# Kernel tuning notes

Measured on AMD Instinct MI355X. Metric: run time of the kernel, lower is better.

Reference implementation:

```python
import jax, jax.numpy as jnp
import numpy as np

B, L = 4096, 200
G_DIM, L_DIM, A_DIM, H = 64, 64, 8, 32
MAX_ACTION = 1.0


def _init(k, shape, fan_in):
    bound = 1.0 / np.sqrt(fan_in)
    return jax.random.uniform(k, shape, jnp.float32, -bound, bound)


def setup_inputs() -> dict:
    key = jax.random.key(0)
    ks = jax.random.split(key, 16)
    return dict(
        global_states=jax.random.normal(ks[0], (B, G_DIM), jnp.float32),
        local_states=jax.random.normal(ks[1], (B, L, L_DIM), jnp.float32),
        W_w=_init(ks[2], (H, G_DIM), G_DIM), W_b=_init(ks[3], (H,), G_DIM),
        U_w=_init(ks[4], (H, L_DIM), L_DIM), U_b=_init(ks[5], (H,), L_DIM),
        att_w=_init(ks[6], (1, 2 * H), 2 * H), att_b=_init(ks[7], (1,), 2 * H),
        l1_w=_init(ks[8], (256, 2 * H), 2 * H), l1_b=_init(ks[9], (256,), 2 * H),
        l2_w=_init(ks[10], (256, 256), 256), l2_b=_init(ks[11], (256,), 256),
        l3_w=_init(ks[12], (A_DIM, 256), 256), l3_b=_init(ks[13], (A_DIM,), 256),
    )


def reference(global_states, local_states, W_w, W_b, U_w, U_b,
              att_w, att_b, l1_w, l1_b, l2_w, l2_b, l3_w, l3_b):
    h = W_w.shape[0]  # 32
    wg = global_states @ W_w.T + W_b                              # [B,H]
    ul = jnp.einsum('bld,hd->blh', local_states, U_w) + U_b       # [B,L,H]
    # att input row0 = cat(wg, wg); rows 1..L = cat(wg, ul)
    a_g, a_l = att_w[0, :h], att_w[0, h:]
    g_term = wg @ a_g                                             # [B]
    s0 = jax.nn.leaky_relu(g_term + wg @ a_l + att_b[0])          # [B]
    sl = jax.nn.leaky_relu(g_term[:, None] + ul @ a_l + att_b[0]) # [B,L]
    # normalize by sum (not softmax), matching torch.div(score, score.sum())
    total = s0 + sl.sum(axis=1)                                   # [B]
    n0 = s0 / total                                               # [B]
    nl = sl / total[:, None]                                      # [B,L]
    agg_local = jnp.einsum('bl,blh->bh', nl, ul)                  # [B,H]
    states = jax.nn.relu(jnp.concatenate([n0[:, None] * wg, agg_local], axis=1))  # [B,2H]
    a = jax.nn.relu(states @ l1_w.T + l1_b)
    a = jax.nn.relu(a @ l2_w.T + l2_b)
    a = jax.nn.sigmoid(a @ l3_w.T + l3_b)
    return MAX_ACTION * a
```

## Files before the change

kernel.cpp:

```cpp
#include <hip/hip_runtime.h>
#include <math.h>

#define BB 4096
#define LL 200
#define GD 64
#define HH 32
#define LPAD 207
#define RR 8

__global__ __launch_bounds__(256) void stage1_kernel(
    const float* __restrict__ gs,
    const float* __restrict__ ls,
    const float* __restrict__ W_w,
    const float* __restrict__ W_b,
    const float* __restrict__ U_w,
    const float* __restrict__ U_b,
    const float* __restrict__ att_w,
    const float* __restrict__ att_b,
    float* __restrict__ states)
{
    __shared__ float xT[64 * LPAD];
    __shared__ float s_wg[HH];
    __shared__ float s_misc[2];
    __shared__ float s_V[HH + 1];

    const int tid = threadIdx.x;
    const int b   = blockIdx.x;

    const float2* ls2 = (const float2*)(ls + (size_t)b * (LL * 64));
    for (int i = tid; i < LL * 32; i += 256) {
        float2 v = ls2[i];
        int d2 = i & 31;
        int l  = i >> 5;
        xT[(2 * d2 + 0) * LPAD + l] = v.x;
        xT[(2 * d2 + 1) * LPAD + l] = v.y;
    }

    if (tid < HH) {
        float acc = W_b[tid];
        const float* g = gs + (size_t)b * GD;
        #pragma unroll
        for (int d = 0; d < GD; ++d)
            acc += g[d] * W_w[tid * GD + d];
        s_wg[tid] = acc;
    }
    __syncthreads();

    const int lx = (tid < LL) ? tid : (LL - 1);
    float x[64];
    #pragma unroll
    for (int d = 0; d < 64; ++d)
        x[d] = xT[d * LPAD + lx];

    if (tid == 0) {
        float gt = 0.f, t2 = 0.f;
        #pragma unroll
        for (int h = 0; h < HH; ++h) {
            gt += s_wg[h] * att_w[h];
            t2 += s_wg[h] * att_w[HH + h];
        }
        float lin = gt + t2 + att_b[0];
        s_misc[0] = gt;
        s_misc[1] = (lin > 0.f) ? lin : 0.01f * lin;
    }
    __syncthreads();

    float* red = xT;
    float t = 0.f;
    for (int h = 0; h < HH; ++h) {
        float acc = U_b[h];
        #pragma unroll
        for (int d = 0; d < 64; ++d)
            acc += x[d] * U_w[h * 64 + d];
        t += acc * att_w[HH + h];
        red[tid * 33 + h] = acc;
    }
    float gt  = s_misc[0];
    float lin = gt + t + att_b[0];
    float sl  = (lin > 0.f) ? lin : 0.01f * lin;
    if (tid >= LL) sl = 0.f;
    red[tid * 33 + 32] = sl;
    __syncthreads();

    if (tid <= HH) {
        float s = 0.f;
        for (int tt = 0; tt < 256; ++tt) {
            float m = (tid < HH) ? red[tt * 33 + tid] : 1.f;
            s += m * red[tt * 33 + 32];
        }
        s_V[tid] = s;
    }
    __syncthreads();

    if (tid < 64) {
        float s0    = s_misc[1];
        float total = s0 + s_V[HH];
        float v;
        if (tid < HH) v = (s0 / total) * s_wg[tid];
        else          v = s_V[tid - HH] / total;
        states[(size_t)b * 64 + tid] = fmaxf(v, 0.f);
    }
}

__global__ __launch_bounds__(256) void mlp_kernel(
    const float* __restrict__ states,
    const float* __restrict__ l1_w, const float* __restrict__ l1_b,
    const float* __restrict__ l2_w, const float* __restrict__ l2_b,
    const float* __restrict__ l3_w, const float* __restrict__ l3_b,
    float* __restrict__ out)
{
    __shared__ __align__(16) float s_x [RR * 64];
    __shared__ __align__(16) float s_a1[RR * 256];
    __shared__ float s_a2[RR * 257];

    const int tid = threadIdx.x;
    const int b0  = blockIdx.x * RR;

    const float4* st4 = (const float4*)(states + (size_t)b0 * 64);
    if (tid < RR * 16) ((float4*)s_x)[tid] = st4[tid];
    __syncthreads();

    float w[64];

    {
        const float* wr = l1_w + tid * 64;
        #pragma unroll
        for (int d = 0; d < 64; ++d) w[d] = wr[d];
        float bias = l1_b[tid];
        #pragma unroll
        for (int r = 0; r < RR; ++r) {
            float acc = bias;
            #pragma unroll
            for (int d = 0; d < 64; ++d)
                acc += s_x[r * 64 + d] * w[d];
            s_a1[r * 256 + tid] = fmaxf(acc, 0.f);
        }
    }
    __syncthreads();

    {
        float acc[RR];
        float bias = l2_b[tid];
        #pragma unroll
        for (int r = 0; r < RR; ++r) acc[r] = bias;
        for (int kc = 0; kc < 4; ++kc) {
            const float* wr = l2_w + tid * 256 + kc * 64;
            #pragma unroll
            for (int d = 0; d < 64; ++d) w[d] = wr[d];
            #pragma unroll
            for (int r = 0; r < RR; ++r) {
                #pragma unroll
                for (int d = 0; d < 64; ++d)
                    acc[r] += s_a1[r * 256 + kc * 64 + d] * w[d];
            }
        }
        #pragma unroll
        for (int r = 0; r < RR; ++r)
            s_a2[r * 257 + tid] = fmaxf(acc[r], 0.f);
    }
    __syncthreads();

    if (tid < RR * 8) {
        int r = tid >> 3, o = tid & 7;
        float acc = l3_b[o];
        const float* wr = l3_w + o * 256;
        #pragma unroll 8
        for (int k = 0; k < 256; ++k)
            acc += s_a2[r * 257 + k] * wr[k];
        out[(size_t)(b0 + r) * 8 + o] = 1.f / (1.f + expf(-acc));
    }
}

extern "C" void kernel_launch(void* const* d_in, const int* in_sizes, int n_in,
                              void* d_out, int out_size, void* d_ws, size_t ws_size,
                              hipStream_t stream)
{
    const float* gs    = (const float*)d_in[0];
    const float* ls    = (const float*)d_in[1];
    const float* W_w   = (const float*)d_in[2];
    const float* W_b   = (const float*)d_in[3];
    const float* U_w   = (const float*)d_in[4];
    const float* U_b   = (const float*)d_in[5];
    const float* att_w = (const float*)d_in[6];
    const float* att_b = (const float*)d_in[7];
    const float* l1_w  = (const float*)d_in[8];
    const float* l1_b  = (const float*)d_in[9];
    const float* l2_w  = (const float*)d_in[10];
    const float* l2_b  = (const float*)d_in[11];
    const float* l3_w  = (const float*)d_in[12];
    const float* l3_b  = (const float*)d_in[13];

    float* states = (float*)d_ws;
    float* out    = (float*)d_out;

    stage1_kernel<<<BB, 256, 0, stream>>>(gs, ls, W_w, W_b, U_w, U_b,
                                          att_w, att_b, states);
    mlp_kernel<<<BB / RR, 256, 0, stream>>>(states, l1_w, l1_b, l2_w, l2_b,
                                            l3_w, l3_b, out);
}
```

Before: 410.8 us.

## Fold attention weights into U and aggregate raw inputs before projecting

The stage-1 kernel is rewritten to use the linearity of the U projection. It precomputes c = a_l·U_w so each score needs only a 64-wide dot product, accumulates the score-weighted sum of raw local states, and applies U_w once per batch row. Each wave now handles one batch row with float4 streaming loads, software prefetch and shuffle reductions, which replaces the shared-memory transpose and the per-position 32x64 projection. The MLP row tile RR is also lowered from 8 to 4, which doubles the number of MLP blocks but reloads the weights more often per row.

```diff
diff --git a/kernel.cpp b/kernel.cpp
--- a/kernel.cpp
+++ b/kernel.cpp
@@ -3,10 +3,8 @@
 
 #define BB 4096
 #define LL 200
-#define GD 64
 #define HH 32
-#define LPAD 207
-#define RR 8
+#define RR 4
 
 __global__ __launch_bounds__(256) void stage1_kernel(
     const float* __restrict__ gs,
@@ -19,87 +17,107 @@
     const float* __restrict__ att_b,
     float* __restrict__ states)
 {
-    __shared__ float xT[64 * LPAD];
-    __shared__ float s_wg[HH];
-    __shared__ float s_misc[2];
-    __shared__ float s_V[HH + 1];
-
-    const int tid = threadIdx.x;
-    const int b   = blockIdx.x;
-
-    const float2* ls2 = (const float2*)(ls + (size_t)b * (LL * 64));
-    for (int i = tid; i < LL * 32; i += 256) {
-        float2 v = ls2[i];
-        int d2 = i & 31;
-        int l  = i >> 5;
-        xT[(2 * d2 + 0) * LPAD + l] = v.x;
-        xT[(2 * d2 + 1) * LPAD + l] = v.y;
-    }
-
-    if (tid < HH) {
-        float acc = W_b[tid];
-        const float* g = gs + (size_t)b * GD;
-        #pragma unroll
-        for (int d = 0; d < GD; ++d)
-            acc += g[d] * W_w[tid * GD + d];
-        s_wg[tid] = acc;
-    }
-    __syncthreads();
-
-    const int lx = (tid < LL) ? tid : (LL - 1);
-    float x[64];
-    #pragma unroll
-    for (int d = 0; d < 64; ++d)
-        x[d] = xT[d * LPAD + lx];
-
-    if (tid == 0) {
-        float gt = 0.f, t2 = 0.f;
-        #pragma unroll
-        for (int h = 0; h < HH; ++h) {
-            gt += s_wg[h] * att_w[h];
-            t2 += s_wg[h] * att_w[HH + h];
-        }
-        float lin = gt + t2 + att_b[0];
-        s_misc[0] = gt;
-        s_misc[1] = (lin > 0.f) ? lin : 0.01f * lin;
-    }
-    __syncthreads();
-
-    float* red = xT;
-    float t = 0.f;
-    for (int h = 0; h < HH; ++h) {
-        float acc = U_b[h];
-        #pragma unroll
-        for (int d = 0; d < 64; ++d)
-            acc += x[d] * U_w[h * 64 + d];
-        t += acc * att_w[HH + h];
-        red[tid * 33 + h] = acc;
-    }
-    float gt  = s_misc[0];
-    float lin = gt + t + att_b[0];
-    float sl  = (lin > 0.f) ? lin : 0.01f * lin;
-    if (tid >= LL) sl = 0.f;
-    red[tid * 33 + 32] = sl;
-    __syncthreads();
-
-    if (tid <= HH) {
-        float s = 0.f;
-        for (int tt = 0; tt < 256; ++tt) {
-            float m = (tid < HH) ? red[tt * 33 + tid] : 1.f;
-            s += m * red[tt * 33 + 32];
-        }
-        s_V[tid] = s;
-    }
-    __syncthreads();
-
-    if (tid < 64) {
-        float s0    = s_misc[1];
-        float total = s0 + s_V[HH];
-        float v;
-        if (tid < HH) v = (s0 / total) * s_wg[tid];
-        else          v = s_V[tid - HH] / total;
-        states[(size_t)b * 64 + tid] = fmaxf(v, 0.f);
-    }
+    __shared__ float c_lds[4 * 64];
+    __shared__ float y_lds[4 * 64];
+
+    const int tid  = threadIdx.x;
+    const int lane = tid & 63;
+    const int wid  = tid >> 6;
+    const int b    = blockIdx.x * 4 + wid;
+
+    const int h    = lane & 31;
+    const int half = lane >> 5;
+    const int q    = lane & 15;
+    const int lg   = lane >> 4;
+
+    const float4* g4 = (const float4*)(gs + (size_t)b * 64);
+    const float4* W4 = (const float4*)(W_w);
+    float wg = (half == 0) ? W_b[h] : 0.f;
+    #pragma unroll
+    for (int dd = 0; dd < 8; ++dd) {
+        float4 gv = g4[half * 8 + dd];
+        float4 wv = W4[h * 16 + half * 8 + dd];
+        wg += gv.x * wv.x + gv.y * wv.y + gv.z * wv.z + gv.w * wv.w;
+    }
+    wg += __shfl_xor(wg, 32);
+
+    float gt = wg * att_w[h];
+    float t2 = wg * att_w[HH + h];
+    #pragma unroll
+    for (int m = 1; m < 32; m <<= 1) {
+        gt += __shfl_xor(gt, m);
+        t2 += __shfl_xor(t2, m);
+    }
+    const float attb = att_b[0];
+    const float lin0 = gt + t2 + attb;
+    const float s0   = (lin0 > 0.f) ? lin0 : 0.01f * lin0;
+
+    float c = 0.f;
+    float ubal = 0.f;
+    #pragma unroll
+    for (int hh = 0; hh < HH; ++hh) {
+        const float alh = att_w[HH + hh];
+        c    += alh * U_w[hh * 64 + lane];
+        ubal += alh * U_b[hh];
+    }
+    c_lds[wid * 64 + lane] = c;
+    __syncthreads();
+    const float4 cq = *(const float4*)&c_lds[wid * 64 + 4 * q];
+    const float base = gt + ubal + attb;
+
+    const float4* xs = (const float4*)(ls + (size_t)b * (LL * 64));
+    const int idx0 = lg * 16 + q;
+    float4 yx = make_float4(0.f, 0.f, 0.f, 0.f);
+    float Sacc = 0.f;
+    float4 X0 = xs[idx0];
+    float4 X1 = xs[idx0 + 64];
+    #pragma unroll 2
+    for (int t = 0; t < 50; ++t) {
+        float4 X = X0;
+        X0 = X1;
+        const int tn = (t + 2 < 50) ? (t + 2) : 49;
+        X1 = xs[idx0 + tn * 64];
+
+        float p = X.x * cq.x + X.y * cq.y + X.z * cq.z + X.w * cq.w;
+        p += __shfl_xor(p, 1);
+        p += __shfl_xor(p, 2);
+        p += __shfl_xor(p, 4);
+        p += __shfl_xor(p, 8);
+        const float linv = p + base;
+        const float sl = (linv > 0.f) ? linv : 0.01f * linv;
+        yx.x += sl * X.x;
+        yx.y += sl * X.y;
+        yx.z += sl * X.z;
+        yx.w += sl * X.w;
+        Sacc += sl;
+    }
+
+    #pragma unroll
+    for (int m = 16; m < 64; m <<= 1) {
+        yx.x += __shfl_xor(yx.x, m);
+        yx.y += __shfl_xor(yx.y, m);
+        yx.z += __shfl_xor(yx.z, m);
+        yx.w += __shfl_xor(yx.w, m);
+        Sacc += __shfl_xor(Sacc, m);
+    }
+    if (lane < 16) *(float4*)&y_lds[wid * 64 + 4 * q] = yx;
+    __syncthreads();
+
+    float V = (half == 0) ? (U_b[h] * Sacc) : 0.f;
+    const float4* U4 = (const float4*)U_w;
+    const float4* y4 = (const float4*)&y_lds[wid * 64];
+    #pragma unroll
+    for (int dd = 0; dd < 8; ++dd) {
+        float4 uv = U4[h * 16 + half * 8 + dd];
+        float4 yv = y4[half * 8 + dd];
+        V += uv.x * yv.x + uv.y * yv.y + uv.z * yv.z + uv.w * yv.w;
+    }
+    V += __shfl_xor(V, 32);
+
+    const float total = s0 + Sacc;
+    const float n0    = s0 / total;
+    const float outv  = (lane < 32) ? (n0 * wg) : (V / total);
+    states[(size_t)b * 64 + lane] = fmaxf(outv, 0.f);
 }
 
 __global__ __launch_bounds__(256) void mlp_kernel(
@@ -193,8 +211,8 @@
     float* states = (float*)d_ws;
     float* out    = (float*)d_out;
 
-    stage1_kernel<<<BB, 256, 0, stream>>>(gs, ls, W_w, W_b, U_w, U_b,
-                                          att_w, att_b, states);
+    stage1_kernel<<<BB / 4, 256, 0, stream>>>(gs, ls, W_w, W_b, U_w, U_b,
+                                              att_w, att_b, states);
     mlp_kernel<<<BB / RR, 256, 0, stream>>>(states, l1_w, l1_b, l2_w, l2_b,
                                             l3_w, l3_b, out);
 }
```

New measurement: 365.6 us. 1.12x faster.
